# Optimization experiments

Hardware: AMD Instinct MI355X
Metric: run time of the kernel (lower is better)

Reference implementation:

```python
import jax, jax.numpy as jnp
import numpy as np

B, L, D, E, N, DDELTA, DCONV = 4, 2048, 1024, 2048, 16, 64, 4
EPS = 1e-5


def setup_inputs() -> dict:
    key = jax.random.key(0)
    ks = jax.random.split(key, 12)
    def rn(k, shape, scale=0.02):
        return (jax.random.normal(k, shape) * scale).astype(jnp.float32)
    return {
        "resid":  jax.random.normal(ks[0], (B, L, D), dtype=jnp.float32),
        "norm_w": jnp.ones((D,), jnp.float32),
        "skip_w": rn(ks[1], (E, D)),          # skip_proj.weight
        "in_w":   rn(ks[2], (E, D)),          # in_proj.weight
        "conv_w": rn(ks[3], (E, 1, DCONV), 0.1),  # depthwise conv1d weight
        "conv_b": jnp.zeros((E,), jnp.float32),
        "Wd1":    rn(ks[4], (DDELTA, E)),     # W_delta_1.weight
        "Wd2_w":  rn(ks[5], (E, DDELTA)),     # W_delta_2.weight
        "Wd2_b":  rn(ks[6], (E,), 0.01),      # W_delta_2.bias
        "WB":     rn(ks[7], (N, E)),          # W_B.weight
        "WC":     rn(ks[8], (N, E)),          # W_C.weight
        "A_log":  (jax.random.normal(ks[9], (E, N)) * 0.5).astype(jnp.float32),
        "W_D":    jnp.ones((E,), jnp.float32),
        "out_w":  rn(ks[10], (D, E)),         # out_proj.weight
    }


def reference(resid, norm_w, skip_w, in_w, conv_w, conv_b, Wd1, Wd2_w, Wd2_b,
              WB, WC, A_log, W_D, out_w):
    # RMSNorm
    x = resid * jax.lax.rsqrt(jnp.mean(resid * resid, axis=-1, keepdims=True) + EPS) * norm_w
    skip = x @ skip_w.T                              # [B,L,E]
    x = x @ in_w.T                                   # [B,L,E]
    # depthwise causal conv1d (padding=DCONV-1 then truncate to L == left-pad only)
    xc = jnp.transpose(x, (0, 2, 1))                 # [B,E,L]
    xc = jax.lax.conv_general_dilated(
        xc, conv_w, window_strides=(1,), padding=[(DCONV - 1, 0)],
        dimension_numbers=("NCH", "OIH", "NCH"), feature_group_count=conv_w.shape[0])
    x = jnp.transpose(xc, (0, 2, 1)) + conv_b        # [B,L,E]
    x = jax.nn.silu(x)                               # ssm input

    A = -jnp.exp(A_log)                              # [E,N]
    delta = jax.nn.softplus((x @ Wd1.T) @ Wd2_w.T + Wd2_b)  # [B,L,E]
    Bm = x @ WB.T                                    # [B,L,N]
    Cm = x @ WC.T                                    # [B,L,N]

    def step(h, inp):
        x_l, d_l, B_l, C_l = inp                     # [B,E],[B,E],[B,N],[B,N]
        A_bar = jnp.exp(d_l[:, :, None] * A)         # [B,E,N]
        h = A_bar * h + (d_l * x_l)[:, :, None] * B_l[:, None, :]
        y_l = jnp.einsum("ben,bn->be", h, C_l)       # h @ C
        return h, y_l

    h0 = jnp.zeros((resid.shape[0], A.shape[0], A.shape[1]), x.dtype)
    xs = (jnp.swapaxes(x, 0, 1), jnp.swapaxes(delta, 0, 1),
          jnp.swapaxes(Bm, 0, 1), jnp.swapaxes(Cm, 0, 1))
    _, ys = jax.lax.scan(step, h0, xs)               # ys: [L,B,E]
    y = jnp.swapaxes(ys, 0, 1)                       # [B,L,E]

    y = y + x * W_D
    y = y * jax.nn.silu(skip)
    y = y @ out_w.T                                  # [B,L,D]
    return resid + y
```

## Files before the change

kernel.cpp:

```cpp
#include <hip/hip_runtime.h>
#include <hip/hip_bf16.h>
#include <math.h>

#define B_ 4
#define L_ 2048
#define D_ 1024
#define E_ 2048
#define N_ 16
#define DD_ 64
#define DCONV_ 4

#define S_SEG 32
#define SEGLEN_ (L_ / S_SEG)

typedef __attribute__((ext_vector_type(8))) short bf16x8;
typedef __attribute__((ext_vector_type(4))) float f32x4;

typedef __attribute__((address_space(1))) const void gvoid_t;
typedef __attribute__((address_space(3))) void lvoid_t;

static __device__ __forceinline__ float silu_f(float x) {
    return x / (1.f + __expf(-x));
}

static __device__ __forceinline__ ushort f2bf(float f) {
    __hip_bfloat16 h = __float2bfloat16(f);
    return *reinterpret_cast<ushort*>(&h);
}

#define LOG2E_ 1.4426950408889634f

__global__ __launch_bounds__(256) void k_rmsnorm_bf(const float* __restrict__ resid,
                                                    const float* __restrict__ nw,
                                                    ushort* __restrict__ out) {
    int row = blockIdx.x;
    const float* r = resid + (size_t)row * D_;
    int t = threadIdx.x;
    float4 v = *reinterpret_cast<const float4*>(&r[t * 4]);
    float ss = v.x * v.x + v.y * v.y + v.z * v.z + v.w * v.w;
#pragma unroll
    for (int o = 32; o >= 1; o >>= 1) ss += __shfl_xor(ss, o, 64);
    __shared__ float red[4];
    if ((t & 63) == 0) red[t >> 6] = ss;
    __syncthreads();
    float tot = red[0] + red[1] + red[2] + red[3];
    float rs = rsqrtf(tot * (1.f / (float)D_) + 1e-5f);
    float4 w4 = *reinterpret_cast<const float4*>(&nw[t * 4]);
    ushort4 o4;
    o4.x = f2bf(v.x * rs * w4.x);
    o4.y = f2bf(v.y * rs * w4.y);
    o4.z = f2bf(v.z * rs * w4.z);
    o4.w = f2bf(v.w * rs * w4.w);
    *reinterpret_cast<ushort4*>(&out[(size_t)row * D_ + t * 4]) = o4;
}

__global__ __launch_bounds__(256) void k_cast_bf(const float* __restrict__ in,
                                                 ushort* __restrict__ out) {
    int i = blockIdx.x * 256 + threadIdx.x;
    float4 v = *reinterpret_cast<const float4*>(&in[i * 4]);
    ushort4 o;
    o.x = f2bf(v.x); o.y = f2bf(v.y); o.z = f2bf(v.z); o.w = f2bf(v.w);
    *reinterpret_cast<ushort4*>(&out[i * 4]) = o;
}

template <int EPI>
__global__ __launch_bounds__(256) void k_gemm_bf(const ushort* __restrict__ A,
                                                 const ushort* __restrict__ W,
                                                 const float* __restrict__ bias,
                                                 const float* __restrict__ addsrc,
                                                 float* __restrict__ C,
                                                 int M, int N, int K) {
    constexpr int BM = 128, BN = 128, BK = 32;
    __shared__ __align__(16) ushort As[BM * BK];
    __shared__ __align__(16) ushort Ws[BN * BK];
    int t = threadIdx.x;
    int m0 = blockIdx.y * BM, n0 = blockIdx.x * BN;
    int wave = t >> 6, lane = t & 63;
    int wr = wave >> 1, wc = wave & 1;
    int lr = lane & 15, lg = lane >> 4;
    int srow = lane >> 2;
    int scol = (lane & 3) * 8;

    f32x4 acc[4][4] = {};

    for (int k0 = 0; k0 < K; k0 += BK) {
#pragma unroll
        for (int p = 0; p < 2; ++p) {
            int seg = wave * 2 + p;
            int row = seg * 16 + srow;
            __builtin_amdgcn_global_load_lds(
                (gvoid_t*)(A + (size_t)(m0 + row) * K + k0 + scol),
                (lvoid_t*)(As + seg * 512), 16, 0, 0);
            __builtin_amdgcn_global_load_lds(
                (gvoid_t*)(W + (size_t)(n0 + row) * K + k0 + scol),
                (lvoid_t*)(Ws + seg * 512), 16, 0, 0);
        }
        __syncthreads();
        bf16x8 af[4], bfr[4];
#pragma unroll
        for (int i = 0; i < 4; ++i) {
            af[i]  = *reinterpret_cast<const bf16x8*>(&As[(wr * 64 + i * 16 + lr) * BK + lg * 8]);
            bfr[i] = *reinterpret_cast<const bf16x8*>(&Ws[(wc * 64 + i * 16 + lr) * BK + lg * 8]);
        }
#pragma unroll
        for (int i = 0; i < 4; ++i)
#pragma unroll
            for (int j = 0; j < 4; ++j)
                acc[i][j] = __builtin_amdgcn_mfma_f32_16x16x32_bf16(af[i], bfr[j], acc[i][j], 0, 0, 0);
        __syncthreads();
    }

#pragma unroll
    for (int i = 0; i < 4; ++i) {
        int mrow = m0 + wr * 64 + i * 16 + lg * 4;
#pragma unroll
        for (int j = 0; j < 4; ++j) {
            int ncol = n0 + wc * 64 + j * 16 + lr;
#pragma unroll
            for (int q = 0; q < 4; ++q) {
                float v = acc[i][j][q];
                size_t idx = (size_t)(mrow + q) * N + ncol;
                if (EPI == 1) {
                    float z = v + bias[ncol];
                    v = (z > 20.f) ? z : log1pf(expf(z));
                }
                if (EPI == 2) v += addsrc[idx];
                C[idx] = v;
            }
        }
    }
}

__global__ __launch_bounds__(256) void k_proj(const ushort* __restrict__ A,
                                              const ushort* __restrict__ Wc,
                                              float* __restrict__ Bm,
                                              float* __restrict__ Cm,
                                              ushort* __restrict__ d1_bf) {
    constexpr int BK = 32, LDB = 40;
    __shared__ __align__(16) ushort As[32 * LDB];
    __shared__ __align__(16) ushort Ws[96 * LDB];
    int t = threadIdx.x;
    int m0 = blockIdx.x * 32;
    int wave = t >> 6, lane = t & 63;
    int rowbase = (wave >> 1) * 16;
    int colbase = (wave & 1) * 48;
    int lr = lane & 15, lg = lane >> 4;

    f32x4 acc[3] = {};

    for (int k0 = 0; k0 < E_; k0 += BK) {
        if (t < 128) {
            int row = t >> 2;
            int cg = (t & 3) * 8;
            *reinterpret_cast<uint4*>(&As[row * LDB + cg]) =
                *reinterpret_cast<const uint4*>(&A[(size_t)(m0 + row) * E_ + k0 + cg]);
        }
        {
            int f = t;
            int row = f >> 2, cg = (f & 3) * 8;
            *reinterpret_cast<uint4*>(&Ws[row * LDB + cg]) =
                *reinterpret_cast<const uint4*>(&Wc[(size_t)row * E_ + k0 + cg]);
            if (t < 128) {
                int f2 = t + 256;
                int row2 = f2 >> 2, cg2 = (f2 & 3) * 8;
                *reinterpret_cast<uint4*>(&Ws[row2 * LDB + cg2]) =
                    *reinterpret_cast<const uint4*>(&Wc[(size_t)row2 * E_ + k0 + cg2]);
            }
        }
        __syncthreads();
        bf16x8 af = *reinterpret_cast<const bf16x8*>(&As[(rowbase + lr) * LDB + lg * 8]);
#pragma unroll
        for (int j = 0; j < 3; ++j) {
            bf16x8 bf = *reinterpret_cast<const bf16x8*>(&Ws[(colbase + j * 16 + lr) * LDB + lg * 8]);
            acc[j] = __builtin_amdgcn_mfma_f32_16x16x32_bf16(af, bf, acc[j], 0, 0, 0);
        }
        __syncthreads();
    }

#pragma unroll
    for (int j = 0; j < 3; ++j) {
        int ncol = colbase + j * 16 + lr;
#pragma unroll
        for (int q = 0; q < 4; ++q) {
            int m = m0 + rowbase + lg * 4 + q;
            float v = acc[j][q];
            if (ncol < 16)      Bm[(size_t)m * 16 + ncol] = v;
            else if (ncol < 32) Cm[(size_t)m * 16 + (ncol - 16)] = v;
            else                d1_bf[(size_t)m * 64 + (ncol - 32)] = f2bf(v);
        }
    }
}

__global__ __launch_bounds__(256) void k_conv_silu(const float* __restrict__ x,
                                                   const float* __restrict__ w,
                                                   const float* __restrict__ bias,
                                                   float* __restrict__ out,
                                                   ushort* __restrict__ out_bf) {
    int idx = blockIdx.x * 256 + threadIdx.x;
    int e = idx & (E_ - 1);
    int l = (idx / E_) & (L_ - 1);
    float4 wv = *reinterpret_cast<const float4*>(&w[e * 4]);
    float acc = bias[e];
    acc = fmaf(wv.w, x[idx], acc);
    if (l >= 1) acc = fmaf(wv.z, x[idx - E_], acc);
    if (l >= 2) acc = fmaf(wv.y, x[idx - 2 * E_], acc);
    if (l >= 3) acc = fmaf(wv.x, x[idx - 3 * E_], acc);
    float s = silu_f(acc);
    out[idx] = s;
    out_bf[idx] = f2bf(s);
}


__global__ __launch_bounds__(256) void k_scan_p1(const float* __restrict__ xs,
                                                 const float* __restrict__ delta,
                                                 const float* __restrict__ Bm,
                                                 const float* __restrict__ A_log,
                                                 float* __restrict__ hbuf,
                                                 float* __restrict__ sdsum) {
    int t = threadIdx.x;
    int bid = blockIdx.x;
    int s = bid & (S_SEG - 1);
    int eblk = (bid >> 5) & 7;
    int b = bid >> 8;
    int e = eblk * 256 + t;

    float A2[16];
#pragma unroll
    for (int i = 0; i < 16; i += 4) {
        f32x4 al = *reinterpret_cast<const f32x4*>(&A_log[(size_t)e * 16 + i]);
#pragma unroll
        for (int j = 0; j < 4; ++j) A2[i + j] = -__expf(al[j]) * LOG2E_;
    }
    f32x4 h4[4] = {};
    float sdl = 0.f;

    const float* dp = delta + ((size_t)b * L_ + s * SEGLEN_) * E_ + e;
    const float* xp = xs    + ((size_t)b * L_ + s * SEGLEN_) * E_ + e;
    const float* Bp = Bm + ((size_t)b * L_ + s * SEGLEN_) * 16;

#pragma unroll 2
    for (int l = 0; l < SEGLEN_; ++l) {
        float d  = dp[(size_t)l * E_];
        float xv = xp[(size_t)l * E_];
        f32x4 B4[4];
#pragma unroll
        for (int g = 0; g < 4; ++g)
            B4[g] = *reinterpret_cast<const f32x4*>(&Bp[l * 16 + g * 4]);
        float dx = d * xv;
        sdl += d;
#pragma unroll
        for (int g = 0; g < 4; ++g) {
            f32x4 e4;
#pragma unroll
            for (int j = 0; j < 4; ++j) e4[j] = exp2f(d * A2[g * 4 + j]);
            h4[g] = e4 * h4[g] + dx * B4[g];
        }
    }
    size_t cidx = ((size_t)(b * S_SEG + s) * E_ + e) * 16;
#pragma unroll
    for (int g = 0; g < 4; ++g)
        *reinterpret_cast<f32x4*>(&hbuf[cidx + g * 4]) = h4[g];
    sdsum[(size_t)(b * S_SEG + s) * E_ + e] = sdl;
}

__global__ __launch_bounds__(256) void k_scan_p2(float* __restrict__ hbuf,
                                                 const float* __restrict__ sdsum,
                                                 const float* __restrict__ A_log) {
    int t = blockIdx.x * 256 + threadIdx.x;
    int q = t & 3;
    int e = (t >> 2) & (E_ - 1);
    int b = t >> 13;
    f32x4 A2;
    {
        f32x4 al = *reinterpret_cast<const f32x4*>(&A_log[(size_t)e * 16 + q * 4]);
#pragma unroll
        for (int i = 0; i < 4; ++i) A2[i] = -__expf(al[i]) * LOG2E_;
    }
    f32x4 acc = {0.f, 0.f, 0.f, 0.f};
    for (int s = 0; s < S_SEG; ++s) {
        size_t idx = ((size_t)(b * S_SEG + s) * E_ + e) * 16 + q * 4;
        f32x4 hl = *reinterpret_cast<const f32x4*>(&hbuf[idx]);
        float sd = sdsum[(size_t)(b * S_SEG + s) * E_ + e];
        *reinterpret_cast<f32x4*>(&hbuf[idx]) = acc;
        f32x4 p;
#pragma unroll
        for (int i = 0; i < 4; ++i) p[i] = exp2f(A2[i] * sd);
        acc = hl + p * acc;
    }
}

__global__ __launch_bounds__(256) void k_scan_p3(const float* __restrict__ xs,
                                                 const float* __restrict__ delta,
                                                 const float* __restrict__ Bm,
                                                 const float* __restrict__ Cm,
                                                 const float* __restrict__ A_log,
                                                 const float* __restrict__ W_D,
                                                 const float* __restrict__ skip,
                                                 const float* __restrict__ hbuf,
                                                 ushort* __restrict__ yg) {
    int t = threadIdx.x;
    int bid = blockIdx.x;
    int s = bid & (S_SEG - 1);
    int eblk = (bid >> 5) & 7;
    int b = bid >> 8;
    int e = eblk * 256 + t;

    float A2[16];
#pragma unroll
    for (int i = 0; i < 16; i += 4) {
        f32x4 al = *reinterpret_cast<const f32x4*>(&A_log[(size_t)e * 16 + i]);
#pragma unroll
        for (int j = 0; j < 4; ++j) A2[i + j] = -__expf(al[j]) * LOG2E_;
    }
    size_t cidx = ((size_t)(b * S_SEG + s) * E_ + e) * 16;
    f32x4 h4[4];
#pragma unroll
    for (int g = 0; g < 4; ++g)
        h4[g] = *reinterpret_cast<const f32x4*>(&hbuf[cidx + g * 4]);
    float wd = W_D[e];

    const float* dp = delta + ((size_t)b * L_ + s * SEGLEN_) * E_ + e;
    const float* xp = xs    + ((size_t)b * L_ + s * SEGLEN_) * E_ + e;
    const float* sp = skip  + ((size_t)b * L_ + s * SEGLEN_) * E_ + e;
    const float* Bp = Bm + ((size_t)b * L_ + s * SEGLEN_) * 16;
    const float* Cp = Cm + ((size_t)b * L_ + s * SEGLEN_) * 16;
    ushort* yp = yg + ((size_t)b * L_ + s * SEGLEN_) * E_ + e;

#pragma unroll 2
    for (int l = 0; l < SEGLEN_; ++l) {
        float d  = dp[(size_t)l * E_];
        float xv = xp[(size_t)l * E_];
        float sk = sp[(size_t)l * E_];
        f32x4 B4[4], C4[4];
#pragma unroll
        for (int g = 0; g < 4; ++g) {
            B4[g] = *reinterpret_cast<const f32x4*>(&Bp[l * 16 + g * 4]);
            C4[g] = *reinterpret_cast<const f32x4*>(&Cp[l * 16 + g * 4]);
        }
        float dx = d * xv;
        f32x4 yv = {0.f, 0.f, 0.f, 0.f};
#pragma unroll
        for (int g = 0; g < 4; ++g) {
            f32x4 e4;
#pragma unroll
            for (int j = 0; j < 4; ++j) e4[j] = exp2f(d * A2[g * 4 + j]);
            h4[g] = e4 * h4[g] + dx * B4[g];
            yv = h4[g] * C4[g] + yv;
        }
        float y = (yv[0] + yv[1]) + (yv[2] + yv[3]);
        float gsk = silu_f(sk);
        yp[(size_t)l * E_] = f2bf((y + xv * wd) * gsk);
    }
}

extern "C" void kernel_launch(void* const* d_in, const int* in_sizes, int n_in,
                              void* d_out, int out_size, void* d_ws, size_t ws_size,
                              hipStream_t stream) {
    const float* resid  = (const float*)d_in[0];
    const float* norm_w = (const float*)d_in[1];
    const float* skip_w = (const float*)d_in[2];
    const float* in_w   = (const float*)d_in[3];
    const float* conv_w = (const float*)d_in[4];
    const float* conv_b = (const float*)d_in[5];
    const float* Wd1    = (const float*)d_in[6];
    const float* Wd2_w  = (const float*)d_in[7];
    const float* Wd2_b  = (const float*)d_in[8];
    const float* WB     = (const float*)d_in[9];
    const float* WC     = (const float*)d_in[10];
    const float* A_log  = (const float*)d_in[11];
    const float* W_D    = (const float*)d_in[12];
    const float* out_w  = (const float*)d_in[13];
    float* out = (float*)d_out;

    const int M = B_ * L_;
    char* p = (char*)d_ws;
    ushort* xn_bf   = (ushort*)p;  p += (size_t)M * D_ * 2;
    ushort* skw_bf  = (ushort*)p;  p += (size_t)E_ * D_ * 2;
    ushort* inw_bf  = (ushort*)p;  p += (size_t)E_ * D_ * 2;
    ushort* outw_bf = (ushort*)p;  p += (size_t)D_ * E_ * 2;
    ushort* yg_bf   = (ushort*)p;  p += (size_t)M * E_ * 2;
    float*  skipb   = (float*)p;   p += (size_t)M * E_ * 4;
    float*  xin     = (float*)p;   p += (size_t)M * E_ * 4;
    float*  xs      = (float*)p;   p += (size_t)M * E_ * 4;
    ushort* d1_bf   = (ushort*)p;  p += (size_t)M * DD_ * 2;
    float*  Bm      = (float*)p;   p += (size_t)M * 16 * 4;
    float*  Cm      = (float*)p;   p += (size_t)M * 16 * 4;
    ushort* wbc_bf  = (ushort*)p;  p += (size_t)96 * E_ * 2;
    ushort* wd2_bf  = (ushort*)p;  p += (size_t)E_ * DD_ * 2;
    float*  delta   = xin;
    ushort* xs_bf   = yg_bf;
    float*  hbuf    = (float*)xn_bf;
    float*  sdsum   = hbuf + (size_t)B_ * S_SEG * E_ * 16;

    dim3 blk(256);

    k_cast_bf<<<dim3((E_ * D_) / 1024), blk, 0, stream>>>(skip_w, skw_bf);
    k_cast_bf<<<dim3((E_ * D_) / 1024), blk, 0, stream>>>(in_w, inw_bf);
    k_cast_bf<<<dim3((D_ * E_) / 1024), blk, 0, stream>>>(out_w, outw_bf);
    k_cast_bf<<<dim3((N_ * E_) / 1024), blk, 0, stream>>>(WB, wbc_bf);
    k_cast_bf<<<dim3((N_ * E_) / 1024), blk, 0, stream>>>(WC, wbc_bf + (size_t)16 * E_);
    k_cast_bf<<<dim3((DD_ * E_) / 1024), blk, 0, stream>>>(Wd1, wbc_bf + (size_t)32 * E_);
    k_cast_bf<<<dim3((E_ * DD_) / 1024), blk, 0, stream>>>(Wd2_w, wd2_bf);
    k_rmsnorm_bf<<<dim3(M), blk, 0, stream>>>(resid, norm_w, xn_bf);
    k_gemm_bf<0><<<dim3(E_ / 128, M / 128), blk, 0, stream>>>(xn_bf, skw_bf, nullptr, nullptr, skipb, M, E_, D_);
    k_gemm_bf<0><<<dim3(E_ / 128, M / 128), blk, 0, stream>>>(xn_bf, inw_bf, nullptr, nullptr, xin, M, E_, D_);
    k_conv_silu<<<dim3((M * E_) / 256), blk, 0, stream>>>(xin, conv_w, conv_b, xs, xs_bf);
    k_proj<<<dim3(M / 32), blk, 0, stream>>>(xs_bf, wbc_bf, Bm, Cm, d1_bf);
    k_gemm_bf<1><<<dim3(E_ / 128, M / 128), blk, 0, stream>>>(d1_bf, wd2_bf, Wd2_b, nullptr, delta, M, E_, DD_);
    k_scan_p1<<<dim3(B_ * S_SEG * (E_ / 256)), blk, 0, stream>>>(xs, delta, Bm, A_log, hbuf, sdsum);
    k_scan_p2<<<dim3((B_ * E_ * 4) / 256), blk, 0, stream>>>(hbuf, sdsum, A_log);
    k_scan_p3<<<dim3(B_ * S_SEG * (E_ / 256)), blk, 0, stream>>>(xs, delta, Bm, Cm, A_log, W_D,
                                                                  skipb, hbuf, yg_bf);
    k_gemm_bf<2><<<dim3(D_ / 128, M / 128), blk, 0, stream>>>(yg_bf, outw_bf, nullptr, resid, out, M, D_, E_);
}
```

Before: 666.3 us.

## Store scan intermediates in bf16, fuse skip/in GEMMs and weight casts

```diff
diff --git a/kernel.cpp b/kernel.cpp
--- a/kernel.cpp
+++ b/kernel.cpp
@@ -26,6 +26,11 @@
 static __device__ __forceinline__ ushort f2bf(float f) {
     __hip_bfloat16 h = __float2bfloat16(f);
     return *reinterpret_cast<ushort*>(&h);
+}
+
+static __device__ __forceinline__ float bf2f(ushort u) {
+    uint v = ((uint)u) << 16;
+    return __uint_as_float(v);
 }
 
 #define LOG2E_ 1.4426950408889634f
@@ -54,13 +59,32 @@
     *reinterpret_cast<ushort4*>(&out[(size_t)row * D_ + t * 4]) = o4;
 }
 
-__global__ __launch_bounds__(256) void k_cast_bf(const float* __restrict__ in,
-                                                 ushort* __restrict__ out) {
+__global__ __launch_bounds__(256) void k_cast_all(const float* __restrict__ skip_w,
+                                                  const float* __restrict__ in_w,
+                                                  const float* __restrict__ out_w,
+                                                  const float* __restrict__ WB,
+                                                  const float* __restrict__ WC,
+                                                  const float* __restrict__ Wd1,
+                                                  const float* __restrict__ Wd2,
+                                                  ushort* __restrict__ w2,
+                                                  ushort* __restrict__ outw,
+                                                  ushort* __restrict__ wbc,
+                                                  ushort* __restrict__ wd2) {
     int i = blockIdx.x * 256 + threadIdx.x;
-    float4 v = *reinterpret_cast<const float4*>(&in[i * 4]);
+    const float* src;
+    ushort* dst;
+    int off;
+    if (i < 524288)       { src = skip_w; dst = w2;            off = i; }
+    else if (i < 1048576) { src = in_w;   dst = w2 + 2097152;  off = i - 524288; }
+    else if (i < 1572864) { src = out_w;  dst = outw;          off = i - 1048576; }
+    else if (i < 1581056) { src = WB;     dst = wbc;           off = i - 1572864; }
+    else if (i < 1589248) { src = WC;     dst = wbc + 32768;   off = i - 1581056; }
+    else if (i < 1622016) { src = Wd1;    dst = wbc + 65536;   off = i - 1589248; }
+    else                  { src = Wd2;    dst = wd2;           off = i - 1622016; }
+    float4 v = *reinterpret_cast<const float4*>(&src[(size_t)off * 4]);
     ushort4 o;
     o.x = f2bf(v.x); o.y = f2bf(v.y); o.z = f2bf(v.z); o.w = f2bf(v.w);
-    *reinterpret_cast<ushort4*>(&out[i * 4]) = o;
+    *reinterpret_cast<ushort4*>(&dst[(size_t)off * 4]) = o;
 }
 
 template <int EPI>
@@ -68,7 +92,8 @@
                                                  const ushort* __restrict__ W,
                                                  const float* __restrict__ bias,
                                                  const float* __restrict__ addsrc,
-                                                 float* __restrict__ C,
+                                                 float* __restrict__ Cf,
+                                                 ushort* __restrict__ Cbf,
                                                  int M, int N, int K) {
     constexpr int BM = 128, BN = 128, BK = 32;
     __shared__ __align__(16) ushort As[BM * BK];
@@ -119,13 +144,22 @@
 #pragma unroll
             for (int q = 0; q < 4; ++q) {
                 float v = acc[i][j][q];
-                size_t idx = (size_t)(mrow + q) * N + ncol;
-                if (EPI == 1) {
+                int m = mrow + q;
+                if (EPI == 0) {
+                    Cf[(size_t)m * N + ncol] = v;
+                } else if (EPI == 1) {
                     float z = v + bias[ncol];
-                    v = (z > 20.f) ? z : log1pf(expf(z));
+                    float r = (z > 20.f) ? z : log1pf(expf(z));
+                    Cbf[(size_t)m * N + ncol] = f2bf(r);
+                } else if (EPI == 2) {
+                    size_t idx = (size_t)m * N + ncol;
+                    Cf[idx] = v + addsrc[idx];
+                } else {
+                    if (ncol < 2048)
+                        Cbf[(size_t)m * 2048 + ncol] = f2bf(v);
+                    else
+                        Cf[(size_t)m * 2048 + (ncol - 2048)] = v;
                 }
-                if (EPI == 2) v += addsrc[idx];
-                C[idx] = v;
             }
         }
     }
@@ -156,8 +190,7 @@
                 *reinterpret_cast<const uint4*>(&A[(size_t)(m0 + row) * E_ + k0 + cg]);
         }
         {
-            int f = t;
-            int row = f >> 2, cg = (f & 3) * 8;
+            int row = t >> 2, cg = (t & 3) * 8;
             *reinterpret_cast<uint4*>(&Ws[row * LDB + cg]) =
                 *reinterpret_cast<const uint4*>(&Wc[(size_t)row * E_ + k0 + cg]);
             if (t < 128) {
@@ -194,7 +227,6 @@
 __global__ __launch_bounds__(256) void k_conv_silu(const float* __restrict__ x,
                                                    const float* __restrict__ w,
                                                    const float* __restrict__ bias,
-                                                   float* __restrict__ out,
                                                    ushort* __restrict__ out_bf) {
     int idx = blockIdx.x * 256 + threadIdx.x;
     int e = idx & (E_ - 1);
@@ -205,18 +237,15 @@
     if (l >= 1) acc = fmaf(wv.z, x[idx - E_], acc);
     if (l >= 2) acc = fmaf(wv.y, x[idx - 2 * E_], acc);
     if (l >= 3) acc = fmaf(wv.x, x[idx - 3 * E_], acc);
-    float s = silu_f(acc);
-    out[idx] = s;
-    out_bf[idx] = f2bf(s);
-}
-
-
-__global__ __launch_bounds__(256) void k_scan_p1(const float* __restrict__ xs,
-                                                 const float* __restrict__ delta,
-                                                 const float* __restrict__ Bm,
-                                                 const float* __restrict__ A_log,
-                                                 float* __restrict__ hbuf,
-                                                 float* __restrict__ sdsum) {
+    out_bf[idx] = f2bf(silu_f(acc));
+}
+
+__global__ __launch_bounds__(256, 4) void k_scan_p1(const ushort* __restrict__ xs,
+                                                    const ushort* __restrict__ delta,
+                                                    const float* __restrict__ Bm,
+                                                    const float* __restrict__ A_log,
+                                                    float* __restrict__ hbuf,
+                                                    float* __restrict__ sdsum) {
     int t = threadIdx.x;
     int bid = blockIdx.x;
     int s = bid & (S_SEG - 1);
@@ -234,28 +263,33 @@
     f32x4 h4[4] = {};
     float sdl = 0.f;
 
-    const float* dp = delta + ((size_t)b * L_ + s * SEGLEN_) * E_ + e;
-    const float* xp = xs    + ((size_t)b * L_ + s * SEGLEN_) * E_ + e;
-    const float* Bp = Bm + ((size_t)b * L_ + s * SEGLEN_) * 16;
-
-#pragma unroll 2
-    for (int l = 0; l < SEGLEN_; ++l) {
-        float d  = dp[(size_t)l * E_];
-        float xv = xp[(size_t)l * E_];
-        f32x4 B4[4];
-#pragma unroll
-        for (int g = 0; g < 4; ++g)
-            B4[g] = *reinterpret_cast<const f32x4*>(&Bp[l * 16 + g * 4]);
+    const ushort* dp = delta + ((size_t)b * L_ + s * SEGLEN_) * E_ + e;
+    const ushort* xp = xs    + ((size_t)b * L_ + s * SEGLEN_) * E_ + e;
+    const float*  Bp = Bm + ((size_t)b * L_ + s * SEGLEN_) * 16;
+
+    auto compute = [&](ushort du, ushort xu, int l) {
+        float d = bf2f(du), xv = bf2f(xu);
         float dx = d * xv;
         sdl += d;
 #pragma unroll
         for (int g = 0; g < 4; ++g) {
+            f32x4 Bv = *reinterpret_cast<const f32x4*>(&Bp[l * 16 + g * 4]);
             f32x4 e4;
 #pragma unroll
             for (int j = 0; j < 4; ++j) e4[j] = exp2f(d * A2[g * 4 + j]);
-            h4[g] = e4 * h4[g] + dx * B4[g];
-        }
-    }
+            h4[g] = e4 * h4[g] + dx * Bv;
+        }
+    };
+
+    ushort duA = dp[0], xuA = xp[0];
+    for (int l = 0; l < SEGLEN_; l += 2) {
+        ushort duB = dp[(l + 1) * E_], xuB = xp[(l + 1) * E_];
+        compute(duA, xuA, l);
+        int ln = l + 2; if (ln > SEGLEN_ - 1) ln = SEGLEN_ - 1;
+        duA = dp[ln * E_]; xuA = xp[ln * E_];
+        compute(duB, xuB, l + 1);
+    }
+
     size_t cidx = ((size_t)(b * S_SEG + s) * E_ + e) * 16;
 #pragma unroll
     for (int g = 0; g < 4; ++g)
@@ -289,15 +323,15 @@
     }
 }
 
-__global__ __launch_bounds__(256) void k_scan_p3(const float* __restrict__ xs,
-                                                 const float* __restrict__ delta,
-                                                 const float* __restrict__ Bm,
-                                                 const float* __restrict__ Cm,
-                                                 const float* __restrict__ A_log,
-                                                 const float* __restrict__ W_D,
-                                                 const float* __restrict__ skip,
-                                                 const float* __restrict__ hbuf,
-                                                 ushort* __restrict__ yg) {
+__global__ __launch_bounds__(256, 4) void k_scan_p3(const ushort* __restrict__ xs,
+                                                    const ushort* __restrict__ delta,
+                                                    const float* __restrict__ Bm,
+                                                    const float* __restrict__ Cm,
+                                                    const float* __restrict__ A_log,
+                                                    const float* __restrict__ W_D,
+                                                    const ushort* __restrict__ skip,
+                                                    const float* __restrict__ hbuf,
+                                                    ushort* __restrict__ yg) {
     int t = threadIdx.x;
     int bid = blockIdx.x;
     int s = bid & (S_SEG - 1);
@@ -319,37 +353,39 @@
         h4[g] = *reinterpret_cast<const f32x4*>(&hbuf[cidx + g * 4]);
     float wd = W_D[e];
 
-    const float* dp = delta + ((size_t)b * L_ + s * SEGLEN_) * E_ + e;
-    const float* xp = xs    + ((size_t)b * L_ + s * SEGLEN_) * E_ + e;
-    const float* sp = skip  + ((size_t)b * L_ + s * SEGLEN_) * E_ + e;
-    const float* Bp = Bm + ((size_t)b * L_ + s * SEGLEN_) * 16;
-    const float* Cp = Cm + ((size_t)b * L_ + s * SEGLEN_) * 16;
+    const ushort* dp = delta + ((size_t)b * L_ + s * SEGLEN_) * E_ + e;
+    const ushort* xp = xs    + ((size_t)b * L_ + s * SEGLEN_) * E_ + e;
+    const ushort* sp = skip  + ((size_t)b * L_ + s * SEGLEN_) * E_ + e;
+    const float*  Bp = Bm + ((size_t)b * L_ + s * SEGLEN_) * 16;
+    const float*  Cp = Cm + ((size_t)b * L_ + s * SEGLEN_) * 16;
     ushort* yp = yg + ((size_t)b * L_ + s * SEGLEN_) * E_ + e;
 
-#pragma unroll 2
-    for (int l = 0; l < SEGLEN_; ++l) {
-        float d  = dp[(size_t)l * E_];
-        float xv = xp[(size_t)l * E_];
-        float sk = sp[(size_t)l * E_];
-        f32x4 B4[4], C4[4];
-#pragma unroll
-        for (int g = 0; g < 4; ++g) {
-            B4[g] = *reinterpret_cast<const f32x4*>(&Bp[l * 16 + g * 4]);
-            C4[g] = *reinterpret_cast<const f32x4*>(&Cp[l * 16 + g * 4]);
-        }
+    auto compute = [&](ushort du, ushort xu, ushort su, int l) {
+        float d = bf2f(du), xv = bf2f(xu);
         float dx = d * xv;
         f32x4 yv = {0.f, 0.f, 0.f, 0.f};
 #pragma unroll
         for (int g = 0; g < 4; ++g) {
+            f32x4 Bv = *reinterpret_cast<const f32x4*>(&Bp[l * 16 + g * 4]);
+            f32x4 Cv = *reinterpret_cast<const f32x4*>(&Cp[l * 16 + g * 4]);
             f32x4 e4;
 #pragma unroll
             for (int j = 0; j < 4; ++j) e4[j] = exp2f(d * A2[g * 4 + j]);
-            h4[g] = e4 * h4[g] + dx * B4[g];
-            yv = h4[g] * C4[g] + yv;
+            h4[g] = e4 * h4[g] + dx * Bv;
+            yv = h4[g] * Cv + yv;
         }
         float y = (yv[0] + yv[1]) + (yv[2] + yv[3]);
-        float gsk = silu_f(sk);
+        float gsk = silu_f(bf2f(su));
         yp[(size_t)l * E_] = f2bf((y + xv * wd) * gsk);
+    };
+
+    ushort duA = dp[0], xuA = xp[0], suA = sp[0];
+    for (int l = 0; l < SEGLEN_; l += 2) {
+        ushort duB = dp[(l + 1) * E_], xuB = xp[(l + 1) * E_], suB = sp[(l + 1) * E_];
+        compute(duA, xuA, suA, l);
+        int ln = l + 2; if (ln > SEGLEN_ - 1) ln = SEGLEN_ - 1;
+        duA = dp[ln * E_]; xuA = xp[ln * E_]; suA = sp[ln * E_];
+        compute(duB, xuB, suB, l + 1);
     }
 }
 
@@ -374,42 +410,37 @@
 
     const int M = B_ * L_;
     char* p = (char*)d_ws;
-    ushort* xn_bf   = (ushort*)p;  p += (size_t)M * D_ * 2;
-    ushort* skw_bf  = (ushort*)p;  p += (size_t)E_ * D_ * 2;
-    ushort* inw_bf  = (ushort*)p;  p += (size_t)E_ * D_ * 2;
-    ushort* outw_bf = (ushort*)p;  p += (size_t)D_ * E_ * 2;
-    ushort* yg_bf   = (ushort*)p;  p += (size_t)M * E_ * 2;
-    float*  skipb   = (float*)p;   p += (size_t)M * E_ * 4;
-    float*  xin     = (float*)p;   p += (size_t)M * E_ * 4;
-    float*  xs      = (float*)p;   p += (size_t)M * E_ * 4;
-    ushort* d1_bf   = (ushort*)p;  p += (size_t)M * DD_ * 2;
-    float*  Bm      = (float*)p;   p += (size_t)M * 16 * 4;
-    float*  Cm      = (float*)p;   p += (size_t)M * 16 * 4;
-    ushort* wbc_bf  = (ushort*)p;  p += (size_t)96 * E_ * 2;
-    ushort* wd2_bf  = (ushort*)p;  p += (size_t)E_ * DD_ * 2;
-    float*  delta   = xin;
-    ushort* xs_bf   = yg_bf;
-    float*  hbuf    = (float*)xn_bf;
-    float*  sdsum   = hbuf + (size_t)B_ * S_SEG * E_ * 16;
+    ushort* xn_bf    = (ushort*)p; p += (size_t)M * D_ * 2;
+    ushort* w2_bf    = (ushort*)p; p += (size_t)2 * E_ * D_ * 2;
+    ushort* outw_bf  = (ushort*)p; p += (size_t)D_ * E_ * 2;
+    ushort* wbc_bf   = (ushort*)p; p += (size_t)96 * E_ * 2;
+    ushort* wd2_bf   = (ushort*)p; p += (size_t)E_ * DD_ * 2;
+    float*  xin      = (float*)p;  p += (size_t)M * E_ * 4;
+    ushort* xs_bf    = (ushort*)p; p += (size_t)M * E_ * 2;
+    ushort* skip_bf  = (ushort*)p; p += (size_t)M * E_ * 2;
+    ushort* delta_bf = (ushort*)p; p += (size_t)M * E_ * 2;
+    ushort* yg_bf    = (ushort*)p; p += (size_t)M * E_ * 2;
+    ushort* d1_bf    = (ushort*)p; p += (size_t)M * DD_ * 2;
+    float*  Bm       = (float*)p;  p += (size_t)M * 16 * 4;
+    float*  Cm       = (float*)p;  p += (size_t)M * 16 * 4;
+    float*  hbuf     = (float*)xin;
+    float*  sdsum    = hbuf + (size_t)B_ * S_SEG * E_ * 16;
 
     dim3 blk(256);
 
-    k_cast_bf<<<dim3((E_ * D_) / 1024), blk, 0, stream>>>(skip_w, skw_bf);
-    k_cast_bf<<<dim3((E_ * D_) / 1024), blk, 0, stream>>>(in_w, inw_bf);
-    k_cast_bf<<<dim3((D_ * E_) / 1024), blk, 0, stream>>>(out_w, outw_bf);
-    k_cast_bf<<<dim3((N_ * E_) / 1024), blk, 0, stream>>>(WB, wbc_bf);
-    k_cast_bf<<<dim3((N_ * E_) / 1024), blk, 0, stream>>>(WC, wbc_bf + (size_t)16 * E_);
-    k_cast_bf<<<dim3((DD_ * E_) / 1024), blk, 0, stream>>>(Wd1, wbc_bf + (size_t)32 * E_);
-    k_cast_bf<<<dim3((E_ * DD_) / 1024), blk, 0, stream>>>(Wd2_w, wd2_bf);
+    k_cast_all<<<dim3(6464), blk, 0, stream>>>(skip_w, in_w, out_w, WB, WC, Wd1, Wd2_w,
+                                               w2_bf, outw_bf, wbc_bf, wd2_bf);
     k_rmsnorm_bf<<<dim3(M), blk, 0, stream>>>(resid, norm_w, xn_bf);
-    k_gemm_bf<0><<<dim3(E_ / 128, M / 128), blk, 0, stream>>>(xn_bf, skw_bf, nullptr, nullptr, skipb, M, E_, D_);
-    k_gemm_bf<0><<<dim3(E_ / 128, M / 128), blk, 0, stream>>>(xn_bf, inw_bf, nullptr, nullptr, xin, M, E_, D_);
-    k_conv_silu<<<dim3((M * E_) / 256), blk, 0, stream>>>(xin, conv_w, conv_b, xs, xs_bf);
+    k_gemm_bf<3><<<dim3(2 * E_ / 128, M / 128), blk, 0, stream>>>(
+        xn_bf, w2_bf, nullptr, nullptr, xin, skip_bf, M, 2 * E_, D_);
+    k_conv_silu<<<dim3((M * E_) / 256), blk, 0, stream>>>(xin, conv_w, conv_b, xs_bf);
     k_proj<<<dim3(M / 32), blk, 0, stream>>>(xs_bf, wbc_bf, Bm, Cm, d1_bf);
-    k_gemm_bf<1><<<dim3(E_ / 128, M / 128), blk, 0, stream>>>(d1_bf, wd2_bf, Wd2_b, nullptr, delta, M, E_, DD_);
-    k_scan_p1<<<dim3(B_ * S_SEG * (E_ / 256)), blk, 0, stream>>>(xs, delta, Bm, A_log, hbuf, sdsum);
+    k_gemm_bf<1><<<dim3(E_ / 128, M / 128), blk, 0, stream>>>(
+        d1_bf, wd2_bf, Wd2_b, nullptr, nullptr, delta_bf, M, E_, DD_);
+    k_scan_p1<<<dim3(B_ * S_SEG * (E_ / 256)), blk, 0, stream>>>(xs_bf, delta_bf, Bm, A_log, hbuf, sdsum);
     k_scan_p2<<<dim3((B_ * E_ * 4) / 256), blk, 0, stream>>>(hbuf, sdsum, A_log);
-    k_scan_p3<<<dim3(B_ * S_SEG * (E_ / 256)), blk, 0, stream>>>(xs, delta, Bm, Cm, A_log, W_D,
-                                                                  skipb, hbuf, yg_bf);
-    k_gemm_bf<2><<<dim3(D_ / 128, M / 128), blk, 0, stream>>>(yg_bf, outw_bf, nullptr, resid, out, M, D_, E_);
-}
+    k_scan_p3<<<dim3(B_ * S_SEG * (E_ / 256)), blk, 0, stream>>>(xs_bf, delta_bf, Bm, Cm, A_log,
+                                                                  W_D, skip_bf, hbuf, yg_bf);
+    k_gemm_bf<2><<<dim3(D_ / 128, M / 128), blk, 0, stream>>>(
+        yg_bf, outw_bf, nullptr, resid, out, nullptr, M, D_, E_);
+}
```

New measurement: 733.0 us. +10.0%, slower.
